# Optimization experiments

Measured on AMD Instinct MI355X. Metric: run time of the kernel, lower is better.

## Reference

```python
import jax, jax.numpy as jnp
import numpy as np

N_NODES = 50000
N_EDGES = 800000
N_GRAPHS = 256
F_IN = 128
H = 64
N_CLASSES = 10


def setup_inputs() -> dict:
    key = jax.random.key(0)
    ks = jax.random.split(key, 12)
    x = jax.random.normal(ks[0], (N_NODES, F_IN), dtype=jnp.float32)
    edge_index = jax.random.randint(ks[1], (2, N_EDGES), 0, N_NODES, dtype=jnp.int64)
    batch = jnp.sort(jax.random.randint(ks[2], (N_NODES,), 0, N_GRAPHS, dtype=jnp.int64))
    def glorot(k, fan_in, fan_out):
        lim = np.sqrt(6.0 / (fan_in + fan_out)).astype(np.float32)
        return jax.random.uniform(k, (fan_in, fan_out), jnp.float32, -lim, lim)
    return {
        "x": x,
        "edge_index": edge_index,
        "batch": batch,
        "W1": glorot(ks[3], F_IN, H), "b1": jnp.zeros((H,), jnp.float32),
        "W2": glorot(ks[4], H, H),    "b2": jnp.zeros((H,), jnp.float32),
        "W3": glorot(ks[5], H, H),    "b3": jnp.zeros((H,), jnp.float32),
        "Wm": glorot(ks[6], H, N_CLASSES), "bm": jnp.zeros((N_CLASSES,), jnp.float32),
    }


def _gcn_norm(edge_index, n_nodes):
    # Add self-loops, unit edge weights, symmetric normalization (PyG gcn_norm).
    loops = jnp.arange(n_nodes, dtype=edge_index.dtype)
    row = jnp.concatenate([edge_index[0], loops])  # source
    col = jnp.concatenate([edge_index[1], loops])  # target (aggregation index)
    deg = jax.ops.segment_sum(jnp.ones_like(col, dtype=jnp.float32), col,
                              num_segments=n_nodes)
    dinv = jnp.where(deg > 0, jax.lax.rsqrt(deg), 0.0)
    norm = dinv[row] * dinv[col]  # [E + N]
    return row, col, norm


def _gcn_conv(x, row, col, norm, W, b, n_nodes):
    h = x @ W                                   # [N, H] dense transform
    msg = h[row] * norm[:, None]                # gather + scale  [E+N, H]
    out = jax.ops.segment_sum(msg, col, num_segments=n_nodes)  # scatter-add
    return out + b


def _l2_normalize(x, eps=1e-12):
    n = jnp.sqrt(jnp.sum(x * x, axis=-1, keepdims=True))
    return x / jnp.maximum(n, eps)


def reference(x, edge_index, batch, W1, b1, W2, b2, W3, b3, Wm, bm):
    n = x.shape[0]
    row, col, norm = _gcn_norm(edge_index, n)
    h = x
    for (W, b) in ((W1, b1), (W2, b2), (W3, b3)):
        h = _gcn_conv(h, row, col, norm, W, b, n)
        h = _l2_normalize(h)       # emb_normalize
        h = jax.nn.relu(h)         # gnn_non_linear
    node_emb = h
    # global_mean_pool over graphs
    sums = jax.ops.segment_sum(h, batch, num_segments=N_GRAPHS)
    counts = jax.ops.segment_sum(jnp.ones((n,), jnp.float32), batch,
                                 num_segments=N_GRAPHS)
    graph_emb = sums / jnp.maximum(counts, 1.0)[:, None]
    logits = graph_emb @ Wm + bm
    probs = jax.nn.softmax(logits, axis=-1)
    return logits, probs, node_emb, graph_emb
```

## Files before the change

kernel.cpp:

```cpp
#include <hip/hip_runtime.h>
#include <math.h>

#define HH 64


__global__ void k_init(int* __restrict__ head, float* __restrict__ sums,
                       int* __restrict__ cursor, int n, int pn) {
    int i = blockIdx.x * blockDim.x + threadIdx.x;
    if (i < n) head[i] = -1;
    if (i < pn) sums[i] = 0.f;
    if (i == 0) *cursor = 0;
}

__global__ void k_link(const int* __restrict__ col, int E,
                       int* __restrict__ head, int* __restrict__ next) {
    int e = blockIdx.x * blockDim.x + threadIdx.x;
    if (e >= E) return;
    int c = col[e];
    int prev = atomicExch(&head[c], e);
    next[e] = prev;
}

template<int FIN>
__global__ __launch_bounds__(256, 3) void k_walk_gemm(const int* __restrict__ row,
                                                      const int* __restrict__ head,
                                                      const int* __restrict__ next,
                                                      int* __restrict__ cursor,
                                                      int* __restrict__ rowptr,
                                                      int* __restrict__ cnt,
                                                      float* __restrict__ dinv,
                                                      int* __restrict__ csr,
                                                      const float* __restrict__ x,
                                                      const float* __restrict__ W,
                                                      float* __restrict__ lin, int n) {
    constexpr int KC = 32;
    constexpr int XS = 68;
    __shared__ __align__(16) float Ws[FIN][HH];
    __shared__ __align__(16) float xs_t[KC][XS];
    const int tid = threadIdx.x;

    {
        int node = blockIdx.x * 256 + tid;
        int lane = tid & 63;
        if (node - tid < n) {
            int len = 0, h = -1;
            if (node < n) {
                h = head[node];
                for (int p = h; p >= 0; p = next[p]) ++len;
                dinv[node] = rsqrtf((float)(len + 1));
            }
            int incl = len;
#pragma unroll
            for (int off = 1; off < 64; off <<= 1) {
                int t = __shfl_up(incl, off, 64);
                if (lane >= off) incl += t;
            }
            int total = __shfl(incl, 63, 64);
            int base = 0;
            if (lane == 0 && total > 0) base = atomicAdd(cursor, total);
            base = __shfl(base, 0, 64);
            int dst = base + incl - len;
            if (node < n) {
                rowptr[node] = dst;
                cnt[node]    = len;
                for (int p = h; p >= 0; p = next[p]) csr[dst++] = row[p];
            }
        }
    }

    const int tx = tid & 15;
    const int ty = tid >> 4;
    const int node0 = blockIdx.x * 64;
    if (node0 >= n) return;

    for (int i = tid * 4; i < FIN * HH; i += 1024)
        *(float4*)&Ws[0][i] = *(const float4*)&W[i];

    float acc[4][4] = {};
    const int rr0 = tid >> 3;
    const int cc  = (tid & 7) * 4;

    for (int kc = 0; kc < FIN; kc += KC) {
        __syncthreads();
        for (int rr = rr0; rr < 64; rr += 32) {
            float4 v = make_float4(0.f, 0.f, 0.f, 0.f);
            if (node0 + rr < n) v = *(const float4*)&x[(size_t)(node0 + rr) * FIN + kc + cc];
            xs_t[cc + 0][rr] = v.x;
            xs_t[cc + 1][rr] = v.y;
            xs_t[cc + 2][rr] = v.z;
            xs_t[cc + 3][rr] = v.w;
        }
        __syncthreads();
#pragma unroll 4
        for (int k = 0; k < KC; ++k) {
            float4 a4 = *(const float4*)&xs_t[k][ty * 4];
            float4 b4 = *(const float4*)&Ws[kc + k][tx * 4];
            acc[0][0] = fmaf(a4.x, b4.x, acc[0][0]);
            acc[0][1] = fmaf(a4.x, b4.y, acc[0][1]);
            acc[0][2] = fmaf(a4.x, b4.z, acc[0][2]);
            acc[0][3] = fmaf(a4.x, b4.w, acc[0][3]);
            acc[1][0] = fmaf(a4.y, b4.x, acc[1][0]);
            acc[1][1] = fmaf(a4.y, b4.y, acc[1][1]);
            acc[1][2] = fmaf(a4.y, b4.z, acc[1][2]);
            acc[1][3] = fmaf(a4.y, b4.w, acc[1][3]);
            acc[2][0] = fmaf(a4.z, b4.x, acc[2][0]);
            acc[2][1] = fmaf(a4.z, b4.y, acc[2][1]);
            acc[2][2] = fmaf(a4.z, b4.z, acc[2][2]);
            acc[2][3] = fmaf(a4.z, b4.w, acc[2][3]);
            acc[3][0] = fmaf(a4.w, b4.x, acc[3][0]);
            acc[3][1] = fmaf(a4.w, b4.y, acc[3][1]);
            acc[3][2] = fmaf(a4.w, b4.z, acc[3][2]);
            acc[3][3] = fmaf(a4.w, b4.w, acc[3][3]);
        }
    }

#pragma unroll
    for (int i = 0; i < 4; ++i) {
        int node = node0 + ty * 4 + i;
        if (node < n) *(float4*)&lin[(size_t)node * HH + tx * 4] = *(float4*)acc[i];
    }
}

template<int FIN>
__global__ __launch_bounds__(256, 4) void k_gemm2(const float* __restrict__ x,
                                                  const float* __restrict__ W,
                                                  const float* __restrict__ dinv,
                                                  float* __restrict__ linS, int n) {
    constexpr int KC = 32;
    constexpr int XS = 68;
    __shared__ __align__(16) float Ws[FIN][HH];
    __shared__ __align__(16) float xs_t[KC][XS];
    const int tid = threadIdx.x;
    const int tx = tid & 15;
    const int ty = tid >> 4;
    const int node0 = blockIdx.x * 64;

    for (int i = tid * 4; i < FIN * HH; i += 1024)
        *(float4*)&Ws[0][i] = *(const float4*)&W[i];

    float acc[4][4] = {};
    const int rr0 = tid >> 3;
    const int cc  = (tid & 7) * 4;

    for (int kc = 0; kc < FIN; kc += KC) {
        __syncthreads();
        for (int rr = rr0; rr < 64; rr += 32) {
            float4 v = make_float4(0.f, 0.f, 0.f, 0.f);
            if (node0 + rr < n) v = *(const float4*)&x[(size_t)(node0 + rr) * FIN + kc + cc];
            xs_t[cc + 0][rr] = v.x;
            xs_t[cc + 1][rr] = v.y;
            xs_t[cc + 2][rr] = v.z;
            xs_t[cc + 3][rr] = v.w;
        }
        __syncthreads();
#pragma unroll 4
        for (int k = 0; k < KC; ++k) {
            float4 a4 = *(const float4*)&xs_t[k][ty * 4];
            float4 b4 = *(const float4*)&Ws[kc + k][tx * 4];
            acc[0][0] = fmaf(a4.x, b4.x, acc[0][0]);
            acc[0][1] = fmaf(a4.x, b4.y, acc[0][1]);
            acc[0][2] = fmaf(a4.x, b4.z, acc[0][2]);
            acc[0][3] = fmaf(a4.x, b4.w, acc[0][3]);
            acc[1][0] = fmaf(a4.y, b4.x, acc[1][0]);
            acc[1][1] = fmaf(a4.y, b4.y, acc[1][1]);
            acc[1][2] = fmaf(a4.y, b4.z, acc[1][2]);
            acc[1][3] = fmaf(a4.y, b4.w, acc[1][3]);
            acc[2][0] = fmaf(a4.z, b4.x, acc[2][0]);
            acc[2][1] = fmaf(a4.z, b4.y, acc[2][1]);
            acc[2][2] = fmaf(a4.z, b4.z, acc[2][2]);
            acc[2][3] = fmaf(a4.z, b4.w, acc[2][3]);
            acc[3][0] = fmaf(a4.w, b4.x, acc[3][0]);
            acc[3][1] = fmaf(a4.w, b4.y, acc[3][1]);
            acc[3][2] = fmaf(a4.w, b4.z, acc[3][2]);
            acc[3][3] = fmaf(a4.w, b4.w, acc[3][3]);
        }
    }

#pragma unroll
    for (int i = 0; i < 4; ++i) {
        int node = node0 + ty * 4 + i;
        if (node < n) {
            float d = dinv[node];
            float4 o = make_float4(acc[i][0] * d, acc[i][1] * d, acc[i][2] * d, acc[i][3] * d);
            *(float4*)&linS[(size_t)node * HH + tx * 4] = o;
        }
    }
}

template<bool WEIGHTED>
__global__ __launch_bounds__(256) void k_gather_q(const float* __restrict__ lin,
                                                  const int* __restrict__ csr,
                                                  const int* __restrict__ rowptr,
                                                  const int* __restrict__ cnt,
                                                  const float* __restrict__ dinv,
                                                  const float* __restrict__ b,
                                                  float* __restrict__ hout, int n) {
    int node = blockIdx.x * 4 + (threadIdx.x >> 6);
    int lane = threadIdx.x & 63;
    if (node >= n) return;
    const int q  = lane >> 4;
    const int fl = (lane & 15) * 4;
    int start = rowptr[node];
    int end = start + cnt[node];
    float di = dinv[node];

    float4 a0 = make_float4(0.f, 0.f, 0.f, 0.f);
    float4 a1 = make_float4(0.f, 0.f, 0.f, 0.f);

    for (int base = start; base < end; base += 64) {
        int m = end - base; if (m > 64) m = 64;
        int idx = base + lane;
        int   sv = (idx < end) ? csr[idx] : 0;
        float wv;
        if (WEIGHTED) wv = (idx < end) ? dinv[sv] : 0.f;
        else          wv = (idx < end) ? 1.f : 0.f;
        for (int j = 0; j < m; j += 16) {
            int l = j + q * 4;
            int   s0 = __shfl(sv, l, 64);
            int   s1 = __shfl(sv, l + 1, 64);
            int   s2 = __shfl(sv, l + 2, 64);
            int   s3 = __shfl(sv, l + 3, 64);
            float w0 = __shfl(wv, l, 64);
            float w1 = __shfl(wv, l + 1, 64);
            float w2 = __shfl(wv, l + 2, 64);
            float w3 = __shfl(wv, l + 3, 64);
            float4 v0 = *(const float4*)&lin[(size_t)s0 * HH + fl];
            float4 v1 = *(const float4*)&lin[(size_t)s1 * HH + fl];
            float4 v2 = *(const float4*)&lin[(size_t)s2 * HH + fl];
            float4 v3 = *(const float4*)&lin[(size_t)s3 * HH + fl];
            a0.x = fmaf(w0, v0.x, a0.x); a0.y = fmaf(w0, v0.y, a0.y);
            a0.z = fmaf(w0, v0.z, a0.z); a0.w = fmaf(w0, v0.w, a0.w);
            a1.x = fmaf(w1, v1.x, a1.x); a1.y = fmaf(w1, v1.y, a1.y);
            a1.z = fmaf(w1, v1.z, a1.z); a1.w = fmaf(w1, v1.w, a1.w);
            a0.x = fmaf(w2, v2.x, a0.x); a0.y = fmaf(w2, v2.y, a0.y);
            a0.z = fmaf(w2, v2.z, a0.z); a0.w = fmaf(w2, v2.w, a0.w);
            a1.x = fmaf(w3, v3.x, a1.x); a1.y = fmaf(w3, v3.y, a1.y);
            a1.z = fmaf(w3, v3.z, a1.z); a1.w = fmaf(w3, v3.w, a1.w);
        }
    }
    float4 acc = make_float4(a0.x + a1.x, a0.y + a1.y, a0.z + a1.z, a0.w + a1.w);
#pragma unroll
    for (int off = 16; off < 64; off <<= 1) {
        acc.x += __shfl_xor(acc.x, off, 64);
        acc.y += __shfl_xor(acc.y, off, 64);
        acc.z += __shfl_xor(acc.z, off, 64);
        acc.w += __shfl_xor(acc.w, off, 64);
    }
    float4 self = *(const float4*)&lin[(size_t)node * HH + fl];
    float sw = WEIGHTED ? di : 1.f;
    acc.x = fmaf(sw, self.x, acc.x);
    acc.y = fmaf(sw, self.y, acc.y);
    acc.z = fmaf(sw, self.z, acc.z);
    acc.w = fmaf(sw, self.w, acc.w);
    float4 b4 = *(const float4*)&b[fl];
    float4 v4 = make_float4(fmaf(di, acc.x, b4.x), fmaf(di, acc.y, b4.y),
                            fmaf(di, acc.z, b4.z), fmaf(di, acc.w, b4.w));
    float ss = v4.x * v4.x + v4.y * v4.y + v4.z * v4.z + v4.w * v4.w;
#pragma unroll
    for (int off = 1; off < 16; off <<= 1) ss += __shfl_xor(ss, off, 64);
    float inv = 1.f / fmaxf(sqrtf(ss), 1e-12f);
    v4.x = fmaxf(v4.x * inv, 0.f);
    v4.y = fmaxf(v4.y * inv, 0.f);
    v4.z = fmaxf(v4.z * inv, 0.f);
    v4.w = fmaxf(v4.w * inv, 0.f);
    if (q == 0) *(float4*)&hout[(size_t)node * HH + fl] = v4;
}

__global__ __launch_bounds__(256) void k_pool(const float* __restrict__ node_emb,
                                              const int* __restrict__ batch,
                                              float* __restrict__ sums,
                                              float* __restrict__ cnts, int n) {
    const int NPW = 16;
    int wave = blockIdx.x * 4 + (threadIdx.x >> 6);
    int lane = threadIdx.x & 63;
    int start = wave * NPW;
    if (start >= n) return;
    int end = start + NPW; if (end > n) end = n;
    int cur = batch[start];
    float acc = 0.f;
    int runlen = 0;
    for (int node = start; node < end; ++node) {
        int g = batch[node];
        if (g != cur) {
            atomicAdd(&sums[(size_t)cur * HH + lane], acc);
            if (lane == 0) atomicAdd(&cnts[cur], (float)runlen);
            acc = 0.f; runlen = 0; cur = g;
        }
        acc += node_emb[(size_t)node * HH + lane];
        ++runlen;
    }
    atomicAdd(&sums[(size_t)cur * HH + lane], acc);
    if (lane == 0) atomicAdd(&cnts[cur], (float)runlen);
}

__global__ void k_final2(const float* __restrict__ sums, const float* __restrict__ cnts,
                         const float* __restrict__ Wm, const float* __restrict__ bm,
                         float* __restrict__ logits, float* __restrict__ probs,
                         float* __restrict__ graph_emb) {
    int g = blockIdx.x;
    int lane = threadIdx.x;
    float mean = sums[(size_t)g * HH + lane] / fmaxf(cnts[g], 1.0f);
    graph_emb[(size_t)g * HH + lane] = mean;

    __shared__ float semb[HH];
    __shared__ float slog[16];
    semb[lane] = mean;
    __syncthreads();
    if (lane < 10) {
        float acc = bm[lane];
        for (int k = 0; k < HH; ++k) acc = fmaf(semb[k], Wm[k * 10 + lane], acc);
        slog[lane] = acc;
    }
    __syncthreads();
    if (lane < 10) {
        float mx = -1e30f;
        for (int j = 0; j < 10; ++j) mx = fmaxf(mx, slog[j]);
        float den = 0.f;
        for (int j = 0; j < 10; ++j) den += __expf(slog[j] - mx);
        float lg = slog[lane];
        logits[g * 10 + lane] = lg;
        probs[g * 10 + lane] = __expf(lg - mx) / den;
    }
}


extern "C" void kernel_launch(void* const* d_in, const int* in_sizes, int n_in,
                              void* d_out, int out_size, void* d_ws, size_t ws_size,
                              hipStream_t stream) {
    const float* x     = (const float*)d_in[0];
    const int*   ei    = (const int*)  d_in[1];
    const int*   batch = (const int*)  d_in[2];
    const float* W1 = (const float*)d_in[3];  const float* b1 = (const float*)d_in[4];
    const float* W2 = (const float*)d_in[5];  const float* b2 = (const float*)d_in[6];
    const float* W3 = (const float*)d_in[7];  const float* b3 = (const float*)d_in[8];
    const float* Wm = (const float*)d_in[9];  const float* bm = (const float*)d_in[10];

    const int N = in_sizes[2];
    const int E = in_sizes[1] / 2;
    const int G = (out_size - N * HH) / (2 * 10 + HH);

    const int* row = ei;
    const int* col = ei + E;

    float* out       = (float*)d_out;
    float* logits    = out;
    float* probs     = out + (size_t)G * 10;
    float* node_emb  = out + (size_t)2 * G * 10;
    float* graph_emb = node_emb + (size_t)N * HH;

    char* w = (char*)d_ws;
    auto alloc = [&](size_t bytes) { char* p = w; w += (bytes + 255) & ~(size_t)255; return p; };
    float* dinv    = (float*)alloc((size_t)N * 4);
    int*   cnt     = (int*)  alloc((size_t)N * 4);
    int*   rowptr  = (int*)  alloc((size_t)N * 4);
    int*   head    = (int*)  alloc((size_t)N * 4);
    int*   nxt     = (int*)  alloc((size_t)E * 4);
    int*   cursor  = (int*)  alloc(256);
    float* sums    = (float*)alloc((size_t)G * HH * 4 + (size_t)G * 4);
    float* cnts    = sums + (size_t)G * HH;
    int*   csr     = (int*)  alloc((size_t)E * 4);
    float* bufA    = (float*)alloc((size_t)N * HH * 4);
    float* bufB    = (float*)alloc((size_t)N * HH * 4);

    const int B = 256;
    dim3 blk(B);
    int node_blocks = (N + 3) / 4;
    int gemm_blocks = (N + 63) / 64;
    int nB = (N + B - 1) / B;
    int eB = (E + B - 1) / B;
    int poolN = G * HH + G;
    int pool_blocks = (N + 63) / 64;

    k_init<<<nB, blk, 0, stream>>>(head, sums, cursor, N, poolN);
    k_link<<<eB, blk, 0, stream>>>(col, E, head, nxt);
    k_walk_gemm<128><<<gemm_blocks, blk, 0, stream>>>(row, head, nxt, cursor, rowptr, cnt,
                                                      dinv, csr, x, W1, bufA, N);

    k_gather_q<true><<<node_blocks, blk, 0, stream>>>(bufA, csr, rowptr, cnt, dinv, b1, bufB, N);
    k_gemm2<64><<<gemm_blocks, blk, 0, stream>>>(bufB, W2, dinv, bufA, N);
    k_gather_q<false><<<node_blocks, blk, 0, stream>>>(bufA, csr, rowptr, cnt, dinv, b2, bufB, N);
    k_gemm2<64><<<gemm_blocks, blk, 0, stream>>>(bufB, W3, dinv, bufA, N);
    k_gather_q<false><<<node_blocks, blk, 0, stream>>>(bufA, csr, rowptr, cnt, dinv, b3, node_emb, N);

    k_pool<<<pool_blocks, blk, 0, stream>>>(node_emb, batch, sums, cnts, N);
    k_final2<<<G, dim3(64), 0, stream>>>(sums, cnts, Wm, bm, logits, probs, graph_emb);
}
```

Before: 307.6 us.

## Build CSR via count/prefix/scatter instead of linked-list walk

Replaces the atomicExch linked-list construction, and the per-node pointer-chasing walk fused into the first GEMM, with a count pass, a wave-level prefix allocation pass and an atomic scatter pass. Pointer chasing through the next array is serial and latency-bound, with heavily divergent trip counts, so the walk is expected to be slow. The new scheme adds two launches and a second set of E atomics. It also makes the neighbour order within each node nondeterministic, which can change float summation order.

Measured after the change: 342.1 us. +11.2%, slower.

```diff
diff --git a/kernel.cpp b/kernel.cpp
--- a/kernel.cpp
+++ b/kernel.cpp
@@ -4,70 +4,65 @@
 #define HH 64
 
 
-__global__ void k_init(int* __restrict__ head, float* __restrict__ sums,
+__global__ void k_init(int* __restrict__ cnt, float* __restrict__ sums,
                        int* __restrict__ cursor, int n, int pn) {
     int i = blockIdx.x * blockDim.x + threadIdx.x;
-    if (i < n) head[i] = -1;
+    if (i < n) cnt[i] = 0;
     if (i < pn) sums[i] = 0.f;
     if (i == 0) *cursor = 0;
 }
 
-__global__ void k_link(const int* __restrict__ col, int E,
-                       int* __restrict__ head, int* __restrict__ next) {
+__global__ void k_count(const int* __restrict__ col, int E, int* __restrict__ cnt) {
+    int e = blockIdx.x * blockDim.x + threadIdx.x;
+    if (e >= E) return;
+    atomicAdd(&cnt[col[e]], 1);
+}
+
+__global__ __launch_bounds__(256) void k_alloc(const int* __restrict__ cnt,
+                                               int* __restrict__ cursor,
+                                               int* __restrict__ rowptr,
+                                               int* __restrict__ wcur,
+                                               float* __restrict__ dinv, int n) {
+    int node = blockIdx.x * blockDim.x + threadIdx.x;
+    int lane = threadIdx.x & 63;
+    if (node - lane >= n) return;
+    int len = (node < n) ? cnt[node] : 0;
+    if (node < n) dinv[node] = rsqrtf((float)(len + 1));
+    int incl = len;
+#pragma unroll
+    for (int off = 1; off < 64; off <<= 1) {
+        int t = __shfl_up(incl, off, 64);
+        if (lane >= off) incl += t;
+    }
+    int total = __shfl(incl, 63, 64);
+    int base = 0;
+    if (lane == 0 && total > 0) base = atomicAdd(cursor, total);
+    base = __shfl(base, 0, 64);
+    int dst = base + incl - len;
+    if (node < n) {
+        rowptr[node] = dst;
+        wcur[node]   = dst;
+    }
+}
+
+__global__ void k_scatter(const int* __restrict__ row, const int* __restrict__ col, int E,
+                          int* __restrict__ wcur, int* __restrict__ csr) {
     int e = blockIdx.x * blockDim.x + threadIdx.x;
     if (e >= E) return;
     int c = col[e];
-    int prev = atomicExch(&head[c], e);
-    next[e] = prev;
-}
-
-template<int FIN>
-__global__ __launch_bounds__(256, 3) void k_walk_gemm(const int* __restrict__ row,
-                                                      const int* __restrict__ head,
-                                                      const int* __restrict__ next,
-                                                      int* __restrict__ cursor,
-                                                      int* __restrict__ rowptr,
-                                                      int* __restrict__ cnt,
-                                                      float* __restrict__ dinv,
-                                                      int* __restrict__ csr,
-                                                      const float* __restrict__ x,
-                                                      const float* __restrict__ W,
-                                                      float* __restrict__ lin, int n) {
+    int dst = atomicAdd(&wcur[c], 1);
+    csr[dst] = row[e];
+}
+
+template<int FIN, bool SCALE>
+__global__ __launch_bounds__(256, (FIN == 128) ? 3 : 4)
+void k_gemm(const float* __restrict__ x, const float* __restrict__ W,
+            const float* __restrict__ dinv, float* __restrict__ out, int n) {
     constexpr int KC = 32;
     constexpr int XS = 68;
     __shared__ __align__(16) float Ws[FIN][HH];
     __shared__ __align__(16) float xs_t[KC][XS];
     const int tid = threadIdx.x;
-
-    {
-        int node = blockIdx.x * 256 + tid;
-        int lane = tid & 63;
-        if (node - tid < n) {
-            int len = 0, h = -1;
-            if (node < n) {
-                h = head[node];
-                for (int p = h; p >= 0; p = next[p]) ++len;
-                dinv[node] = rsqrtf((float)(len + 1));
-            }
-            int incl = len;
-#pragma unroll
-            for (int off = 1; off < 64; off <<= 1) {
-                int t = __shfl_up(incl, off, 64);
-                if (lane >= off) incl += t;
-            }
-            int total = __shfl(incl, 63, 64);
-            int base = 0;
-            if (lane == 0 && total > 0) base = atomicAdd(cursor, total);
-            base = __shfl(base, 0, 64);
-            int dst = base + incl - len;
-            if (node < n) {
-                rowptr[node] = dst;
-                cnt[node]    = len;
-                for (int p = h; p >= 0; p = next[p]) csr[dst++] = row[p];
-            }
-        }
-    }
-
     const int tx = tid & 15;
     const int ty = tid >> 4;
     const int node0 = blockIdx.x * 64;
@@ -117,72 +112,15 @@
 #pragma unroll
     for (int i = 0; i < 4; ++i) {
         int node = node0 + ty * 4 + i;
-        if (node < n) *(float4*)&lin[(size_t)node * HH + tx * 4] = *(float4*)acc[i];
-    }
-}
-
-template<int FIN>
-__global__ __launch_bounds__(256, 4) void k_gemm2(const float* __restrict__ x,
-                                                  const float* __restrict__ W,
-                                                  const float* __restrict__ dinv,
-                                                  float* __restrict__ linS, int n) {
-    constexpr int KC = 32;
-    constexpr int XS = 68;
-    __shared__ __align__(16) float Ws[FIN][HH];
-    __shared__ __align__(16) float xs_t[KC][XS];
-    const int tid = threadIdx.x;
-    const int tx = tid & 15;
-    const int ty = tid >> 4;
-    const int node0 = blockIdx.x * 64;
-
-    for (int i = tid * 4; i < FIN * HH; i += 1024)
-        *(float4*)&Ws[0][i] = *(const float4*)&W[i];
-
-    float acc[4][4] = {};
-    const int rr0 = tid >> 3;
-    const int cc  = (tid & 7) * 4;
-
-    for (int kc = 0; kc < FIN; kc += KC) {
-        __syncthreads();
-        for (int rr = rr0; rr < 64; rr += 32) {
-            float4 v = make_float4(0.f, 0.f, 0.f, 0.f);
-            if (node0 + rr < n) v = *(const float4*)&x[(size_t)(node0 + rr) * FIN + kc + cc];
-            xs_t[cc + 0][rr] = v.x;
-            xs_t[cc + 1][rr] = v.y;
-            xs_t[cc + 2][rr] = v.z;
-            xs_t[cc + 3][rr] = v.w;
-        }
-        __syncthreads();
-#pragma unroll 4
-        for (int k = 0; k < KC; ++k) {
-            float4 a4 = *(const float4*)&xs_t[k][ty * 4];
-            float4 b4 = *(const float4*)&Ws[kc + k][tx * 4];
-            acc[0][0] = fmaf(a4.x, b4.x, acc[0][0]);
-            acc[0][1] = fmaf(a4.x, b4.y, acc[0][1]);
-            acc[0][2] = fmaf(a4.x, b4.z, acc[0][2]);
-            acc[0][3] = fmaf(a4.x, b4.w, acc[0][3]);
-            acc[1][0] = fmaf(a4.y, b4.x, acc[1][0]);
-            acc[1][1] = fmaf(a4.y, b4.y, acc[1][1]);
-            acc[1][2] = fmaf(a4.y, b4.z, acc[1][2]);
-            acc[1][3] = fmaf(a4.y, b4.w, acc[1][3]);
-            acc[2][0] = fmaf(a4.z, b4.x, acc[2][0]);
-            acc[2][1] = fmaf(a4.z, b4.y, acc[2][1]);
-            acc[2][2] = fmaf(a4.z, b4.z, acc[2][2]);
-            acc[2][3] = fmaf(a4.z, b4.w, acc[2][3]);
-            acc[3][0] = fmaf(a4.w, b4.x, acc[3][0]);
-            acc[3][1] = fmaf(a4.w, b4.y, acc[3][1]);
-            acc[3][2] = fmaf(a4.w, b4.z, acc[3][2]);
-            acc[3][3] = fmaf(a4.w, b4.w, acc[3][3]);
-        }
-    }
-
-#pragma unroll
-    for (int i = 0; i < 4; ++i) {
-        int node = node0 + ty * 4 + i;
         if (node < n) {
-            float d = dinv[node];
-            float4 o = make_float4(acc[i][0] * d, acc[i][1] * d, acc[i][2] * d, acc[i][3] * d);
-            *(float4*)&linS[(size_t)node * HH + tx * 4] = o;
+            if (SCALE) {
+                float d = dinv[node];
+                float4 o = make_float4(acc[i][0] * d, acc[i][1] * d,
+                                       acc[i][2] * d, acc[i][3] * d);
+                *(float4*)&out[(size_t)node * HH + tx * 4] = o;
+            } else {
+                *(float4*)&out[(size_t)node * HH + tx * 4] = *(float4*)acc[i];
+            }
         }
     }
 }
@@ -353,8 +291,7 @@
     float* dinv    = (float*)alloc((size_t)N * 4);
     int*   cnt     = (int*)  alloc((size_t)N * 4);
     int*   rowptr  = (int*)  alloc((size_t)N * 4);
-    int*   head    = (int*)  alloc((size_t)N * 4);
-    int*   nxt     = (int*)  alloc((size_t)E * 4);
+    int*   wcur    = (int*)  alloc((size_t)N * 4);
     int*   cursor  = (int*)  alloc(256);
     float* sums    = (float*)alloc((size_t)G * HH * 4 + (size_t)G * 4);
     float* cnts    = sums + (size_t)G * HH;
@@ -371,15 +308,16 @@
     int poolN = G * HH + G;
     int pool_blocks = (N + 63) / 64;
 
-    k_init<<<nB, blk, 0, stream>>>(head, sums, cursor, N, poolN);
-    k_link<<<eB, blk, 0, stream>>>(col, E, head, nxt);
-    k_walk_gemm<128><<<gemm_blocks, blk, 0, stream>>>(row, head, nxt, cursor, rowptr, cnt,
-                                                      dinv, csr, x, W1, bufA, N);
-
+    k_init<<<nB, blk, 0, stream>>>(cnt, sums, cursor, N, poolN);
+    k_count<<<eB, blk, 0, stream>>>(col, E, cnt);
+    k_alloc<<<nB, blk, 0, stream>>>(cnt, cursor, rowptr, wcur, dinv, N);
+    k_scatter<<<eB, blk, 0, stream>>>(row, col, E, wcur, csr);
+
+    k_gemm<128, false><<<gemm_blocks, blk, 0, stream>>>(x, W1, dinv, bufA, N);
     k_gather_q<true><<<node_blocks, blk, 0, stream>>>(bufA, csr, rowptr, cnt, dinv, b1, bufB, N);
-    k_gemm2<64><<<gemm_blocks, blk, 0, stream>>>(bufB, W2, dinv, bufA, N);
+    k_gemm<64, true><<<gemm_blocks, blk, 0, stream>>>(bufB, W2, dinv, bufA, N);
     k_gather_q<false><<<node_blocks, blk, 0, stream>>>(bufA, csr, rowptr, cnt, dinv, b2, bufB, N);
-    k_gemm2<64><<<gemm_blocks, blk, 0, stream>>>(bufB, W3, dinv, bufA, N);
+    k_gemm<64, true><<<gemm_blocks, blk, 0, stream>>>(bufB, W3, dinv, bufA, N);
     k_gather_q<false><<<node_blocks, blk, 0, stream>>>(bufA, csr, rowptr, cnt, dinv, b3, node_emb, N);
 
     k_pool<<<pool_blocks, blk, 0, stream>>>(node_emb, batch, sums, cnts, N);
```
